# Optimization experiments

Hardware: AMD Instinct MI355X
Metric: run time of the kernel (lower is better)

The kernel has to match this reference:

```python
import jax, jax.numpy as jnp
import numpy as np

NEG = -1e30  # effective -inf in float32, safe under logaddexp grads
EPS = 1e-7   # keras.backend.epsilon()


def _ctc_loss(y_pred, y_true):
    """Faithful port of keras.backend.ctc_batch_cost with full-length
    input_length=T and label_length=L (as the CTCLayer sets them).
    y_pred: [B, T, C] post-softmax probabilities; blank = C-1.
    y_true: [B, L] int labels in [0, C-1).
    Returns loss [B, 1].
    """
    logp = jnp.log(y_pred + EPS)            # keras takes log(prob + eps)
    B, T, C = y_pred.shape
    L = y_true.shape[1]
    S = 2 * L + 1
    blank = C - 1

    # Extended label sequence: blank, l1, blank, l2, ..., blank  -> [B, S]
    ext = jnp.full((B, S), blank, dtype=y_true.dtype).at[:, 1::2].set(y_true)
    # Per-time emission log-probs of extended symbols: [B, T, S]
    lp_ext = jnp.take_along_axis(logp, ext[:, None, :], axis=2)

    # Skip transition s-2 -> s allowed when ext[s] != blank and ext[s] != ext[s-2]
    prev2_ext = jnp.pad(ext[:, :-2], ((0, 0), (2, 0)), constant_values=-1)
    allow_skip = (ext != blank) & (ext != prev2_ext)  # [B, S]

    # alpha init at t=0
    alpha = jnp.full((B, S), NEG, dtype=logp.dtype)
    alpha = alpha.at[:, 0].set(lp_ext[:, 0, 0]).at[:, 1].set(lp_ext[:, 0, 1])

    def step(alpha, lp_t):
        shift1 = jnp.pad(alpha[:, :-1], ((0, 0), (1, 0)), constant_values=NEG)
        shift2 = jnp.pad(alpha[:, :-2], ((0, 0), (2, 0)), constant_values=NEG)
        shift2 = jnp.where(allow_skip, shift2, NEG)
        new = jnp.logaddexp(jnp.logaddexp(alpha, shift1), shift2) + lp_t
        return new, None

    lp_seq = jnp.moveaxis(lp_ext[:, 1:, :], 1, 0)  # [T-1, B, S]
    alpha, _ = jax.lax.scan(step, alpha, lp_seq)

    # Terminate in final blank or final label
    loss = -jnp.logaddexp(alpha[:, S - 1], alpha[:, S - 2])  # [B]
    return loss[:, None]  # keras returns [B, 1]


def setup_inputs() -> dict:
    key = jax.random.key(0)
    k1, k2 = jax.random.split(key)
    B, T, C, L = 256, 256, 1000, 64
    y_true = jax.random.randint(k1, (B, L), 0, C - 1, dtype=jnp.int64)
    logits = jax.random.normal(k2, (B, T, C), dtype=jnp.float32)
    y_pred = jax.nn.softmax(logits, axis=-1)  # module expects softmax probs
    return {"y_true": y_true, "y_pred": y_pred}


def reference(y_true, y_pred):
    return _ctc_loss(y_pred, y_true)
```

## Files before the change

### kernel.cpp

```cpp
#include <hip/hip_runtime.h>


#define T_   256
#define C_   1000
#define L_   64
#define S_   129
#define BLANK 999
#define NEGF (-1e30f)
#define EPSF (1e-7f)

__device__ __forceinline__ float lae2(float a, float b) {
    float m = fmaxf(a, b);
    return m + __logf(__expf(a - m) + __expf(b - m));
}

__global__ __launch_bounds__(192)
void ctc_fwd_kernel(const int* __restrict__ y_true,
                    const float* __restrict__ y_pred,
                    float* __restrict__ out) {
    const int b = blockIdx.x;
    const int s = threadIdx.x;

    __shared__ float buf[2][S_ + 3];
    __shared__ int   lab[L_];

    if (s < L_) lab[s] = y_true[b * L_ + s];
    __syncthreads();

    const float* __restrict__ yp = y_pred + (size_t)b * T_ * C_;

    int  extlab = BLANK;
    bool allow  = false;
    if (s < S_ && (s & 1)) {
        extlab = lab[s >> 1];
        allow  = (s >= 3) && (extlab != lab[(s >> 1) - 1]);
    }

    if (s < S_) {
        float a = NEGF;
        if (s == 0) a = __logf(yp[BLANK]  + EPSF);
        if (s == 1) a = __logf(yp[extlab] + EPSF);
        buf[0][s] = a;
    }
    int cur = 0;

    float gA[4], gB[4];

    auto loadG = [&](float (&g)[4], int tb) {
        #pragma unroll
        for (int i = 0; i < 4; ++i) {
            int t = tb + i;
            if (t > T_ - 1) t = T_ - 1;
            g[i] = (s < S_) ? yp[t * C_ + extlab] : 0.0f;
        }
    };
    auto consume = [&](float (&g)[4], int tb) {
        #pragma unroll
        for (int i = 0; i < 4; ++i) {
            int t = tb + i;
            if (t < T_) {
                __syncthreads();
                if (s < S_) {
                    float a  = buf[cur][s];
                    float a1 = (s >= 1) ? buf[cur][s - 1] : NEGF;
                    float a2 = (s >= 2 && allow) ? buf[cur][s - 2] : NEGF;
                    float m  = fmaxf(fmaxf(a, a1), a2);
                    float r  = __expf(a - m) + __expf(a1 - m) + __expf(a2 - m);
                    float lp = __logf(g[i] + EPSF);
                    buf[cur ^ 1][s] = m + __logf(r) + lp;
                }
                cur ^= 1;
            }
        }
    };

    loadG(gA, 1);
    for (int t0 = 1; t0 < T_; t0 += 8) {
        loadG(gB, t0 + 4);
        consume(gA, t0);
        loadG(gA, t0 + 8);
        consume(gB, t0 + 4);
    }

    __syncthreads();
    if (s == 0) {
        out[b] = -lae2(buf[cur][S_ - 1], buf[cur][S_ - 2]);
    }
}

extern "C" void kernel_launch(void* const* d_in, const int* in_sizes, int n_in,
                              void* d_out, int out_size, void* d_ws, size_t ws_size,
                              hipStream_t stream) {
    const int*   y_true = (const int*)d_in[0];
    const float* y_pred = (const float*)d_in[1];
    float*       out    = (float*)d_out;
    (void)in_sizes; (void)n_in; (void)d_ws; (void)ws_size; (void)out_size;

    ctc_fwd_kernel<<<dim3(256), dim3(192), 0, stream>>>(y_true, y_pred, out);
}
```

Baseline: 395.2 us.

## Run CTC alpha recursion in one wavefront with register state and shuffles

Replaces the 192-thread block that kept alpha in shared memory behind a barrier every step with a single 64-lane wavefront. Each lane owns one label plus its preceding blank (and lane 63 also the final blank), and neighbour values come from __shfl_up instead of shared memory. Emission probabilities are prefetched 8 steps ahead in registers. This removes per-step __syncthreads and LDS traffic on the serial critical path, at the cost of more transcendental work per lane and a fixed assumption that L equals the wavefront width.

```diff
diff --git a/kernel.cpp b/kernel.cpp
--- a/kernel.cpp
+++ b/kernel.cpp
@@ -1,90 +1,81 @@
 #include <hip/hip_runtime.h>
 
 
-#define T_   256
-#define C_   1000
-#define L_   64
-#define S_   129
+#define T_    256
+#define C_    1000
+#define L_    64
 #define BLANK 999
-#define NEGF (-1e30f)
-#define EPSF (1e-7f)
+#define NEGF  (-1e30f)
+#define EPSF  (1e-7f)
+#define PD    8
 
-__device__ __forceinline__ float lae2(float a, float b) {
-    float m = fmaxf(a, b);
-    return m + __logf(__expf(a - m) + __expf(b - m));
-}
-
-__global__ __launch_bounds__(192)
+__global__ __launch_bounds__(64)
 void ctc_fwd_kernel(const int* __restrict__ y_true,
                     const float* __restrict__ y_pred,
                     float* __restrict__ out) {
-    const int b = blockIdx.x;
-    const int s = threadIdx.x;
-
-    __shared__ float buf[2][S_ + 3];
-    __shared__ int   lab[L_];
-
-    if (s < L_) lab[s] = y_true[b * L_ + s];
-    __syncthreads();
+    const int b    = blockIdx.x;
+    const int lane = threadIdx.x;
 
     const float* __restrict__ yp = y_pred + (size_t)b * T_ * C_;
 
-    int  extlab = BLANK;
-    bool allow  = false;
-    if (s < S_ && (s & 1)) {
-        extlab = lab[s >> 1];
-        allow  = (s >= 3) && (extlab != lab[(s >> 1) - 1]);
+    const int lab   = y_true[b * L_ + lane];
+    const int labm1 = __shfl_up(lab, 1, 64);
+    const bool allow = (lane > 0) && (lab != labm1);
+
+    float aE, aO, aL;
+    {
+        float pb = yp[BLANK];
+        float pl = yp[lab];
+        aE = (lane == 0) ? __logf(pb + EPSF) : NEGF;
+        aO = (lane == 0) ? __logf(pl + EPSF) : NEGF;
+        aL = NEGF;
     }
 
-    if (s < S_) {
-        float a = NEGF;
-        if (s == 0) a = __logf(yp[BLANK]  + EPSF);
-        if (s == 1) a = __logf(yp[extlab] + EPSF);
-        buf[0][s] = a;
-    }
-    int cur = 0;
-
-    float gA[4], gB[4];
-
-    auto loadG = [&](float (&g)[4], int tb) {
-        #pragma unroll
-        for (int i = 0; i < 4; ++i) {
-            int t = tb + i;
-            if (t > T_ - 1) t = T_ - 1;
-            g[i] = (s < S_) ? yp[t * C_ + extlab] : 0.0f;
-        }
-    };
-    auto consume = [&](float (&g)[4], int tb) {
-        #pragma unroll
-        for (int i = 0; i < 4; ++i) {
-            int t = tb + i;
-            if (t < T_) {
-                __syncthreads();
-                if (s < S_) {
-                    float a  = buf[cur][s];
-                    float a1 = (s >= 1) ? buf[cur][s - 1] : NEGF;
-                    float a2 = (s >= 2 && allow) ? buf[cur][s - 2] : NEGF;
-                    float m  = fmaxf(fmaxf(a, a1), a2);
-                    float r  = __expf(a - m) + __expf(a1 - m) + __expf(a2 - m);
-                    float lp = __logf(g[i] + EPSF);
-                    buf[cur ^ 1][s] = m + __logf(r) + lp;
-                }
-                cur ^= 1;
-            }
-        }
-    };
-
-    loadG(gA, 1);
-    for (int t0 = 1; t0 < T_; t0 += 8) {
-        loadG(gB, t0 + 4);
-        consume(gA, t0);
-        loadG(gA, t0 + 8);
-        consume(gB, t0 + 4);
+    float pbB[PD], pbL[PD];
+    #pragma unroll
+    for (int k = 0; k < PD; ++k) {
+        int t = 1 + k; if (t > T_ - 1) t = T_ - 1;
+        const float* p = yp + t * C_;
+        pbB[k] = p[BLANK];
+        pbL[k] = p[lab];
     }
 
-    __syncthreads();
-    if (s == 0) {
-        out[b] = -lae2(buf[cur][S_ - 1], buf[cur][S_ - 2]);
+    for (int tb = 1; tb < T_; tb += PD) {
+        #pragma unroll
+        for (int j = 0; j < PD; ++j) {
+            const int t = tb + j;
+            if (t >= T_) break;
+
+            int tn = t + PD; if (tn > T_ - 1) tn = T_ - 1;
+            const float* pn = yp + tn * C_;
+            float nB = pn[BLANK];
+            float nL = pn[lab];
+
+            const float lpB = __logf(pbB[j] + EPSF);
+            const float lpL = __logf(pbL[j] + EPSF);
+
+            float upO = __shfl_up(aO, 1, 64);
+            if (lane == 0) upO = NEGF;
+
+            float mE = fmaxf(aE, upO);
+            float nE = mE + __logf(__expf(aE - mE) + __expf(upO - mE)) + lpB;
+
+            float sk = allow ? upO : NEGF;
+            float mO = fmaxf(fmaxf(aO, aE), sk);
+            float nO = mO + __logf(__expf(aO - mO) + __expf(aE - mO) +
+                                   __expf(sk - mO)) + lpL;
+
+            float mL = fmaxf(aL, aO);
+            float nL2 = mL + __logf(__expf(aL - mL) + __expf(aO - mL)) + lpB;
+
+            aE = nE; aO = nO; aL = nL2;
+            pbB[j] = nB; pbL[j] = nL;
+        }
+    }
+
+    if (lane == 63) {
+        float m = fmaxf(aL, aO);
+        out[b] = -(m + __logf(__expf(aL - m) + __expf(aO - m)));
     }
 }
 
@@ -96,5 +87,5 @@
     float*       out    = (float*)d_out;
     (void)in_sizes; (void)n_in; (void)d_ws; (void)ws_size; (void)out_size;
 
-    ctc_fwd_kernel<<<dim3(256), dim3(192), 0, stream>>>(y_true, y_pred, out);
+    ctc_fwd_kernel<<<dim3(256), dim3(64), 0, stream>>>(y_true, y_pred, out);
 }
```

Result: faster. 382.8 us (-3.2%).
